# Kernel tuning notes

Measured on AMD Instinct MI355X. Metric: run time of the kernel, lower is better.

Reference implementation:

```python
import jax, jax.numpy as jnp
import numpy as np
from math import sqrt

B, NQ, NK = 16, 1024, 1024
DIM_Q = DIM_K = DIM_V = 512
H = 8
EPS = 1e-5


def _layernorm(x, gamma, beta):
    mu = jnp.mean(x, axis=-1, keepdims=True)
    var = jnp.mean(jnp.square(x - mu), axis=-1, keepdims=True)
    return (x - mu) * jax.lax.rsqrt(var + EPS) * gamma + beta


def setup_inputs() -> dict:
    key = jax.random.key(0)
    ks = jax.random.split(key, 12)
    s = 0.02
    return {
        "Q": jax.random.normal(ks[0], (B, NQ, DIM_Q), jnp.float32),
        "K": jax.random.normal(ks[1], (B, NK, DIM_K), jnp.float32),
        "Wq": jax.random.normal(ks[2], (DIM_Q, DIM_V), jnp.float32) * s,
        "bq": jnp.zeros((DIM_V,), jnp.float32),
        "Wk": jax.random.normal(ks[3], (DIM_K, DIM_V), jnp.float32) * s,
        "bk": jnp.zeros((DIM_V,), jnp.float32),
        "Wv": jax.random.normal(ks[4], (DIM_K, DIM_V), jnp.float32) * s,
        "bv": jnp.zeros((DIM_V,), jnp.float32),
        "Wo": jax.random.normal(ks[5], (DIM_V, DIM_V), jnp.float32) * s,
        "bo": jnp.zeros((DIM_V,), jnp.float32),
        "g0": jnp.ones((DIM_V,), jnp.float32),
        "b0": jnp.zeros((DIM_V,), jnp.float32),
        "g1": jnp.ones((DIM_V,), jnp.float32),
        "b1": jnp.zeros((DIM_V,), jnp.float32),
    }


def reference(Q, K, Wq, bq, Wk, bk, Wv, bv, Wo, bo, g0, b0, g1, b1):
    d = DIM_V // H  # head dim
    q = (Q @ Wq + bq).reshape(B, NQ, H, d)
    k = (K @ Wk + bk).reshape(B, NK, H, d)
    v = (K @ Wv + bv).reshape(B, NK, H, d)
    # NOTE: original scales by sqrt(dim_V), not sqrt(head_dim)
    scores = jnp.einsum("bqhd,bkhd->bhqk", q, k) / sqrt(DIM_V)
    A = jax.nn.softmax(scores, axis=-1)
    attn = jnp.einsum("bhqk,bkhd->bqhd", A, v)
    O = (q + attn).reshape(B, NQ, DIM_V)  # residual is post-projection q
    O = _layernorm(O, g0, b0)
    O = O + jax.nn.relu(O @ Wo + bo)
    O = _layernorm(O, g1, b1)
    return O
```

## Files before the change

### kernel.cpp

```cpp
#include <hip/hip_runtime.h>
#include <hip/hip_bf16.h>

typedef __attribute__((ext_vector_type(8))) short short8;
typedef __attribute__((ext_vector_type(4))) float f32x4;
typedef __attribute__((ext_vector_type(4))) float float4v;
typedef __attribute__((ext_vector_type(4))) unsigned short ushort4v;
typedef __attribute__((ext_vector_type(4))) unsigned int uint4v;
typedef __attribute__((ext_vector_type(2))) unsigned int uint2v;

#define MFMA16(a, b, c) __builtin_amdgcn_mfma_f32_16x16x32_bf16((a), (b), (c), 0, 0, 0)

__device__ __forceinline__ unsigned short f2bf(float f) {
    union { float f; unsigned u; } v; v.f = f;
    unsigned r = v.u + 0x7fffu + ((v.u >> 16) & 1u);
    return (unsigned short)(r >> 16);
}
__device__ __forceinline__ float bf2f(unsigned short h) {
    union { unsigned u; float f; } v; v.u = (unsigned)h << 16;
    return v.f;
}
__device__ __forceinline__ float asf(unsigned u) {
    union { unsigned u; float f; } v; v.u = u;
    return v.f;
}
__device__ __forceinline__ unsigned cvt_pk_bf16(float lo, float hi) {
    unsigned r;
    asm("v_cvt_pk_bf16_f32 %0, %1, %2" : "=v"(r) : "v"(lo), "v"(hi));
    return r;
}
__device__ __forceinline__ void gl16(const void* g, void* l) {
    __builtin_amdgcn_global_load_lds(
        (const __attribute__((address_space(1))) unsigned int*)g,
        (__attribute__((address_space(3))) unsigned int*)l, 16, 0, 0);
}

__global__ __launch_bounds__(256) void wtrans_kernel(
    const float* __restrict__ W0, const float* __restrict__ W1,
    const float* __restrict__ W2, const float* __restrict__ W3,
    unsigned short* __restrict__ T0, unsigned short* __restrict__ T1,
    unsigned short* __restrict__ T2, unsigned short* __restrict__ T3)
{
    const int z = blockIdx.z;
    const float* W = (z == 0) ? W0 : (z == 1) ? W1 : (z == 2) ? W2 : W3;
    unsigned short* T = (z == 0) ? T0 : (z == 1) ? T1 : (z == 2) ? T2 : T3;

    __shared__ unsigned short tile[64][72];
    const int k0 = blockIdx.x * 64, n0 = blockIdx.y * 64;
    const int t = threadIdx.x;

#pragma unroll
    for (int p = 0; p < 4; ++p) {
        int idx = p * 256 + t;
        int k = idx >> 4, c4 = idx & 15;
        float4v v = *(const float4v*)(W + (size_t)(k0 + k) * 512 + n0 + c4 * 4);
#pragma unroll
        for (int j = 0; j < 4; ++j) tile[k][c4 * 4 + j] = f2bf(v[j]);
    }
    __syncthreads();
#pragma unroll
    for (int p = 0; p < 2; ++p) {
        int idx = p * 256 + t;
        int n = idx >> 3, c = idx & 7;
        short8 o;
#pragma unroll
        for (int j = 0; j < 8; ++j) o[j] = (short)tile[c * 8 + j][n];
        *(short8*)(T + (size_t)(n0 + n) * 512 + k0 + ((c ^ (n & 7)) * 8)) = o;
    }
}

__global__ __launch_bounds__(256) void proj_kernel(
    const float* __restrict__ Q, const float* __restrict__ Kin,
    const unsigned short* __restrict__ WqT, const unsigned short* __restrict__ WkT,
    const unsigned short* __restrict__ WvT,
    const float* __restrict__ bq, const float* __restrict__ bk, const float* __restrict__ bv,
    unsigned short* __restrict__ qb, unsigned short* __restrict__ kb,
    unsigned short* __restrict__ vT)
{
    const int bid = blockIdx.x;
    const int xcd = bid & 7, idx = bid >> 3;
    const int q12 = idx / 12, combo = idx - q12 * 12;
    const int z = combo >> 2;
    const int rowbase = (xcd + 8 * q12) * 128;
    const int colbase = (combo & 3) * 128;

    const float* A = (z == 0) ? Q : Kin;
    const unsigned short* WT = (z == 0) ? WqT : (z == 1) ? WkT : WvT;
    const float* bias = (z == 0) ? bq : (z == 1) ? bk : bv;

    __shared__ float Alf[128 * 64];
    __shared__ unsigned short Bl[128 * 64];

    const int t = threadIdx.x;
    const int lane = t & 63, wid = t >> 6;
    const int wm = wid >> 1, wn = wid & 1;
    const int l15 = lane & 15, grp = lane >> 4;
    const int srow = t >> 3, sblk = t & 7;

    f32x4 acc[4][4];
#pragma unroll
    for (int i = 0; i < 4; ++i)
#pragma unroll
        for (int j = 0; j < 4; ++j) acc[i][j] = (f32x4){0.f, 0.f, 0.f, 0.f};

    for (int kt = 0; kt < 8; ++kt) {
#pragma unroll
        for (int p = 0; p < 4; ++p)
            gl16(WT + (size_t)(colbase + p * 32 + srow) * 512 + kt * 64 + sblk * 8,
                 &Bl[p * 2048 + wid * 512]);
#pragma unroll
        for (int i = 0; i < 8; ++i) {
            int r = wid * 32 + i * 4 + (lane >> 4);
            int cdst = lane & 15;
            gl16(A + (size_t)(rowbase + r) * 512 + kt * 64 + ((cdst ^ (r & 15)) << 2),
                 &Alf[wid * 2048 + i * 256]);
        }
        __syncthreads();
#pragma unroll
        for (int kk = 0; kk < 2; ++kk) {
            short8 af[4], bfr[4];
#pragma unroll
            for (int m = 0; m < 4; ++m) {
                int r = wm * 64 + m * 16 + l15;
                int c0 = kk * 8 + grp * 2;
                float4v f0 = *(const float4v*)((const char*)Alf + r * 256 + ((c0 ^ (r & 15)) << 4));
                float4v f1 = *(const float4v*)((const char*)Alf + r * 256 + (((c0 + 1) ^ (r & 15)) << 4));
                union { uint4v u; short8 s8; } cv;
                cv.u[0] = cvt_pk_bf16(f0[0], f0[1]);
                cv.u[1] = cvt_pk_bf16(f0[2], f0[3]);
                cv.u[2] = cvt_pk_bf16(f1[0], f1[1]);
                cv.u[3] = cvt_pk_bf16(f1[2], f1[3]);
                af[m] = cv.s8;
            }
#pragma unroll
            for (int n = 0; n < 4; ++n) {
                int r = wn * 64 + n * 16 + l15;
                bfr[n] = *(const short8*)((const char*)Bl + r * 128 + (((kk * 4 + grp) ^ (r & 7)) << 4));
            }
#pragma unroll
            for (int m = 0; m < 4; ++m)
#pragma unroll
                for (int n = 0; n < 4; ++n)
                    acc[m][n] = MFMA16(af[m], bfr[n], acc[m][n]);
        }
        __syncthreads();
    }

    if (z == 2) {
#pragma unroll
        for (int n = 0; n < 4; ++n) {
            int col = colbase + wn * 64 + n * 16 + l15;
            float bvv = bias[col];
            int h_ = col >> 6, d_ = col & 63;
#pragma unroll
            for (int m = 0; m < 4; ++m) {
                int row0 = rowbase + wm * 64 + m * 16 + grp * 4;
                int b_ = row0 >> 10;
                int key0 = row0 & 1023;
                int keypos = (key0 & ~63) + ((((key0 >> 3) & 7) ^ (d_ & 7)) << 3) + (key0 & 7);
                ushort4v w;
#pragma unroll
                for (int r = 0; r < 4; ++r) w[r] = f2bf(acc[m][n][r] + bvv);
                *(ushort4v*)(vT + ((size_t)(b_ * 8 + h_) * 64 + d_) * 1024 + keypos) = w;
            }
        }
    } else if (z == 1) {
#pragma unroll
        for (int n = 0; n < 4; ++n) {
            int col = colbase + wn * 64 + n * 16 + l15;
            float bvv = bias[col];
#pragma unroll
            for (int m = 0; m < 4; ++m) {
                int row0 = rowbase + wm * 64 + m * 16 + grp * 4;
#pragma unroll
                for (int r = 0; r < 4; ++r) {
                    int row = row0 + r;
                    int k6 = row & 63;
                    int y = ((k6 & 4) << 3) | ((k6 & 56) >> 1) | (k6 & 3);
                    int Y = (row & ~63) | y;
                    int colp = col ^ ((y & 7) << 3);
                    kb[(size_t)Y * 512 + colp] = f2bf(acc[m][n][r] + bvv);
                }
            }
        }
    } else {
#pragma unroll
        for (int n = 0; n < 4; ++n) {
            int col = colbase + wn * 64 + n * 16 + l15;
            float bvv = bias[col];
#pragma unroll
            for (int m = 0; m < 4; ++m) {
                int row0 = rowbase + wm * 64 + m * 16 + grp * 4;
#pragma unroll
                for (int r = 0; r < 4; ++r)
                    qb[(size_t)(row0 + r) * 512 + col] = f2bf(acc[m][n][r] + bvv);
            }
        }
    }
}

__global__ __launch_bounds__(256, 4) void attn_kernel(
    const unsigned short* __restrict__ qb, const unsigned short* __restrict__ kbs,
    const unsigned short* __restrict__ vTs, unsigned short* __restrict__ Opre)
{
    __shared__ unsigned short Kl[2][64 * 64];
    __shared__ unsigned short Vl[2][64 * 64];

    const int t = threadIdx.x, lane = t & 63, wid = t >> 6;
    const int l15 = lane & 15, grp = lane >> 4;

    const int bid = blockIdx.x;
    const int h = bid & 7, r2 = bid >> 3;
    const int b = r2 >> 3, qt = r2 & 7;
    const int qbase = qt * 128 + wid * 32;

    const unsigned short* ksrc = kbs + (size_t)(b * 1024 + (t >> 3)) * 512 + h * 64 + (t & 7) * 8;
    const unsigned short* vsrc = vTs + ((size_t)(b * 8 + h) * 64 + (t >> 3)) * 1024 + (t & 7) * 8;

#define STAGE(bsel, tile) do { \
    gl16(ksrc + (size_t)((tile) * 64) * 512,      &Kl[bsel][wid * 512]); \
    gl16(ksrc + (size_t)((tile) * 64 + 32) * 512, &Kl[bsel][2048 + wid * 512]); \
    gl16(vsrc + (tile) * 64,                      &Vl[bsel][wid * 512]); \
    gl16(vsrc + 32768 + (tile) * 64,              &Vl[bsel][2048 + wid * 512]); } while (0)

    const float C = 0.06375871f;

    short8 qfrag[2][2];
#pragma unroll
    for (int qf = 0; qf < 2; ++qf)
#pragma unroll
        for (int kk = 0; kk < 2; ++kk)
            qfrag[qf][kk] = *(const short8*)(
                qb + (size_t)(b * 1024 + qbase + qf * 16 + l15) * 512 + h * 64 + kk * 32 + grp * 8);

    STAGE(0, 0);

#pragma unroll
    for (int qf = 0; qf < 2; ++qf)
#pragma unroll
        for (int kk = 0; kk < 2; ++kk) {
            union { short8 s; uint4v u; } io;
            io.s = qfrag[qf][kk];
#pragma unroll
            for (int j = 0; j < 4; ++j) {
                unsigned w = io.u[j];
                float flo = asf(w << 16) * C;
                float fhi = asf(w & 0xffff0000u) * C;
                io.u[j] = cvt_pk_bf16(flo, fhi);
            }
            qfrag[qf][kk] = io.s;
        }

    f32x4 o[2][4];
#pragma unroll
    for (int qf = 0; qf < 2; ++qf)
#pragma unroll
        for (int df = 0; df < 4; ++df) o[qf][df] = (f32x4){0.f, 0.f, 0.f, 0.f};
    float mrun[2] = {0.f, 0.f}, lrun[2] = {0.f, 0.f};

    __syncthreads();

    for (int kt = 0; kt < 16; ++kt) {
        const int buf = kt & 1;
        if (kt < 15) STAGE(buf ^ 1, kt + 1);

        const char* Kb_ = (const char*)&Kl[buf][0];
        const char* Vb_ = (const char*)&Vl[buf][0];

        f32x4 s[2][4];
#pragma unroll
        for (int qf = 0; qf < 2; ++qf)
#pragma unroll
            for (int nf = 0; nf < 4; ++nf) s[qf][nf] = (f32x4){0.f, 0.f, 0.f, 0.f};
        __builtin_amdgcn_s_setprio(1);
#pragma unroll
        for (int kk = 0; kk < 2; ++kk) {
            short8 kf[4];
#pragma unroll
            for (int nf = 0; nf < 4; ++nf) {
                int r = nf * 16 + l15;
                kf[nf] = *(const short8*)(Kb_ + r * 128 + (((kk * 4 + grp) ^ (r & 7)) << 4));
            }
#pragma unroll
            for (int qf = 0; qf < 2; ++qf)
#pragma unroll
                for (int nf = 0; nf < 4; ++nf)
                    s[qf][nf] = MFMA16(kf[nf], qfrag[qf][kk], s[qf][nf]);
        }
        __builtin_amdgcn_s_setprio(0);

        short8 pa[2][2];
#pragma unroll
        for (int qf = 0; qf < 2; ++qf) {
            float a0 = fmaxf(fmaxf(s[qf][0][0], s[qf][0][1]), fmaxf(s[qf][0][2], s[qf][0][3]));
            float a1 = fmaxf(fmaxf(s[qf][1][0], s[qf][1][1]), fmaxf(s[qf][1][2], s[qf][1][3]));
            float a2 = fmaxf(fmaxf(s[qf][2][0], s[qf][2][1]), fmaxf(s[qf][2][2], s[qf][2][3]));
            float a3 = fmaxf(fmaxf(s[qf][3][0], s[qf][3][1]), fmaxf(s[qf][3][2], s[qf][3][3]));
            float lm = fmaxf(fmaxf(a0, a1), fmaxf(a2, a3));
            if (__any(lm - mrun[qf] > 8.f)) {
                float mr = lm;
                mr = fmaxf(mr, __shfl_xor(mr, 16));
                mr = fmaxf(mr, __shfl_xor(mr, 32));
                float mnew = fmaxf(mrun[qf], mr);
                float rs = __builtin_amdgcn_exp2f(mrun[qf] - mnew);
                mrun[qf] = mnew;
                lrun[qf] *= rs;
#pragma unroll
                for (int df = 0; df < 4; ++df)
#pragma unroll
                    for (int r = 0; r < 4; ++r) o[qf][df][r] *= rs;
            }
            float p[4][4];
            const float mq = mrun[qf];
            if (mq == 0.f) {
#pragma unroll
                for (int nf = 0; nf < 4; ++nf)
#pragma unroll
                    for (int r = 0; r < 4; ++r)
                        p[nf][r] = __builtin_amdgcn_exp2f(s[qf][nf][r]);
            } else {
#pragma unroll
                for (int nf = 0; nf < 4; ++nf)
#pragma unroll
                    for (int r = 0; r < 4; ++r)
                        p[nf][r] = __builtin_amdgcn_exp2f(s[qf][nf][r] - mq);
            }
            float t0 = (p[0][0] + p[0][1]) + (p[0][2] + p[0][3]);
            float t1 = (p[1][0] + p[1][1]) + (p[1][2] + p[1][3]);
            float t2 = (p[2][0] + p[2][1]) + (p[2][2] + p[2][3]);
            float t3 = (p[3][0] + p[3][1]) + (p[3][2] + p[3][3]);
            lrun[qf] += (t0 + t1) + (t2 + t3);
            union { uint4v u; short8 s8; } c0, c1;
            c0.u[0] = cvt_pk_bf16(p[0][0], p[0][1]);
            c0.u[1] = cvt_pk_bf16(p[0][2], p[0][3]);
            c0.u[2] = cvt_pk_bf16(p[2][0], p[2][1]);
            c0.u[3] = cvt_pk_bf16(p[2][2], p[2][3]);
            c1.u[0] = cvt_pk_bf16(p[1][0], p[1][1]);
            c1.u[1] = cvt_pk_bf16(p[1][2], p[1][3]);
            c1.u[2] = cvt_pk_bf16(p[3][0], p[3][1]);
            c1.u[3] = cvt_pk_bf16(p[3][2], p[3][3]);
            pa[qf][0] = c0.s8;
            pa[qf][1] = c1.s8;
        }

        __builtin_amdgcn_s_setprio(1);
#pragma unroll
        for (int kk = 0; kk < 2; ++kk)
#pragma unroll
            for (int df = 0; df < 4; ++df) {
                int r = df * 16 + l15;
                short8 vf = *(const short8*)(Vb_ + r * 128 + (((kk * 4 + grp) ^ (r & 7)) << 4));
#pragma unroll
                for (int qf = 0; qf < 2; ++qf)
                    o[qf][df] = MFMA16(vf, pa[qf][kk], o[qf][df]);
            }
        __builtin_amdgcn_s_setprio(0);
        __syncthreads();
    }
#undef STAGE

#pragma unroll
    for (int qf = 0; qf < 2; ++qf) {
        float l = lrun[qf];
        l += __shfl_xor(l, 16);
        l += __shfl_xor(l, 32);
        float linv = 1.f / l;
        size_t row = (size_t)(b * 1024 + qbase + qf * 16 + l15);
#pragma unroll
        for (int df = 0; df < 4; ++df) {
            int col = h * 64 + df * 16 + grp * 4;
            ushort4v res = *(const ushort4v*)(qb + row * 512 + col);
            ushort4v outv;
#pragma unroll
            for (int r = 0; r < 4; ++r)
                outv[r] = f2bf(o[qf][df][r] * linv + bf2f(res[r]));
            *(ushort4v*)(Opre + row * 512 + col) = outv;
        }
    }
}

template <int OUT_F32>
__global__ __launch_bounds__(256) void ln_kernel(
    const unsigned short* in, const float* __restrict__ g, const float* __restrict__ be,
    unsigned short* outb, float* outf)
{
    const int wid = threadIdx.x >> 6, lane = threadIdx.x & 63;
    const size_t row = (size_t)blockIdx.x * 4 + wid;
    short8 v = *(const short8*)(in + row * 512 + lane * 8);
    float x[8];
    float sum = 0.f, sq = 0.f;
#pragma unroll
    for (int j = 0; j < 8; ++j) {
        x[j] = bf2f((unsigned short)v[j]);
        sum += x[j];
        sq += x[j] * x[j];
    }
#pragma unroll
    for (int ofs = 1; ofs < 64; ofs <<= 1) {
        sum += __shfl_xor(sum, ofs);
        sq += __shfl_xor(sq, ofs);
    }
    float mean = sum * (1.f / 512.f);
    float var = sq * (1.f / 512.f) - mean * mean;
    float rs = rsqrtf(var + 1e-5f);
    float4v g0 = *(const float4v*)(g + lane * 8);
    float4v g1 = *(const float4v*)(g + lane * 8 + 4);
    float4v b0 = *(const float4v*)(be + lane * 8);
    float4v b1 = *(const float4v*)(be + lane * 8 + 4);
    float y[8];
#pragma unroll
    for (int j = 0; j < 4; ++j) y[j] = (x[j] - mean) * rs * g0[j] + b0[j];
#pragma unroll
    for (int j = 0; j < 4; ++j) y[4 + j] = (x[4 + j] - mean) * rs * g1[j] + b1[j];
    if (OUT_F32) {
        float4v o0, o1;
#pragma unroll
        for (int j = 0; j < 4; ++j) { o0[j] = y[j]; o1[j] = y[4 + j]; }
        *(float4v*)(outf + row * 512 + lane * 8) = o0;
        *(float4v*)(outf + row * 512 + lane * 8 + 4) = o1;
    } else {
        short8 o;
#pragma unroll
        for (int j = 0; j < 8; ++j) o[j] = (short)f2bf(y[j]);
        size_t op = row * 512 + (size_t)((lane >> 3) * 64 + (((lane & 7) ^ ((int)row & 7)) * 8));
        *(short8*)(outb + op) = o;
    }
}

__global__ __launch_bounds__(256) void ffn_kernel(
    const unsigned short* __restrict__ O1, const unsigned short* __restrict__ WoT,
    const float* __restrict__ bo, unsigned short* __restrict__ O2)
{
    __shared__ unsigned short Al[128 * 64];
    __shared__ unsigned short Bl[128 * 64];

    const int bid = blockIdx.x;
    const int xcd = bid & 7, idx = bid >> 3;
    const int rowbase = (xcd + 8 * (idx >> 2)) * 128;
    const int colbase = (idx & 3) * 128;

    const int t = threadIdx.x;
    const int lane = t & 63, wid = t >> 6;
    const int wm = wid >> 1, wn = wid & 1;
    const int l15 = lane & 15, grp = lane >> 4;
    const int srow = t >> 3, sblk = t & 7;

    f32x4 acc[4][4];
#pragma unroll
    for (int i = 0; i < 4; ++i)
#pragma unroll
        for (int j = 0; j < 4; ++j) acc[i][j] = (f32x4){0.f, 0.f, 0.f, 0.f};

    for (int kt = 0; kt < 8; ++kt) {
#pragma unroll
        for (int p = 0; p < 4; ++p)
            gl16(O1 + (size_t)(rowbase + p * 32 + srow) * 512 + kt * 64 + sblk * 8,
                 &Al[p * 2048 + wid * 512]);
#pragma unroll
        for (int p = 0; p < 4; ++p)
            gl16(WoT + (size_t)(colbase + p * 32 + srow) * 512 + kt * 64 + sblk * 8,
                 &Bl[p * 2048 + wid * 512]);
        __syncthreads();
#pragma unroll
        for (int kk = 0; kk < 2; ++kk) {
            short8 af[4], bfr[4];
#pragma unroll
            for (int m = 0; m < 4; ++m) {
                int r = wm * 64 + m * 16 + l15;
                af[m] = *(const short8*)((const char*)Al + r * 128 + (((kk * 4 + grp) ^ (r & 7)) << 4));
            }
#pragma unroll
            for (int n = 0; n < 4; ++n) {
                int r = wn * 64 + n * 16 + l15;
                bfr[n] = *(const short8*)((const char*)Bl + r * 128 + (((kk * 4 + grp) ^ (r & 7)) << 4));
            }
#pragma unroll
            for (int m = 0; m < 4; ++m)
#pragma unroll
                for (int n = 0; n < 4; ++n)
                    acc[m][n] = MFMA16(af[m], bfr[n], acc[m][n]);
        }
        __syncthreads();
    }
#pragma unroll
    for (int n = 0; n < 4; ++n) {
        int col = colbase + wn * 64 + n * 16 + l15;
        float bvv = bo[col];
#pragma unroll
        for (int m = 0; m < 4; ++m) {
            int row0 = rowbase + wm * 64 + m * 16 + grp * 4;
#pragma unroll
            for (int r = 0; r < 4; ++r) {
                size_t row = (size_t)(row0 + r);
                float val = fmaxf(acc[m][n][r] + bvv, 0.f);
                float resid = bf2f(O1[row * 512 + (col ^ (((int)row & 7) << 3))]);
                O2[row * 512 + col] = f2bf(resid + val);
            }
        }
    }
}

extern "C" void kernel_launch(void* const* d_in, const int* in_sizes, int n_in,
                              void* d_out, int out_size, void* d_ws, size_t ws_size,
                              hipStream_t stream)
{
    const float* Q   = (const float*)d_in[0];
    const float* Kin = (const float*)d_in[1];
    const float* Wq  = (const float*)d_in[2];
    const float* bq  = (const float*)d_in[3];
    const float* Wk  = (const float*)d_in[4];
    const float* bk  = (const float*)d_in[5];
    const float* Wv  = (const float*)d_in[6];
    const float* bv  = (const float*)d_in[7];
    const float* Wo  = (const float*)d_in[8];
    const float* bo  = (const float*)d_in[9];
    const float* g0  = (const float*)d_in[10];
    const float* b0  = (const float*)d_in[11];
    const float* g1  = (const float*)d_in[12];
    const float* b1  = (const float*)d_in[13];
    float* out = (float*)d_out;

    unsigned short* ws = (unsigned short*)d_ws;
    const size_t WSZ = 512 * 512;
    const size_t BIG = 16384 * 512;
    unsigned short* WqT  = ws;
    unsigned short* WkT  = WqT + WSZ;
    unsigned short* WvT  = WkT + WSZ;
    unsigned short* WoT  = WvT + WSZ;
    unsigned short* qb   = WoT + WSZ;
    unsigned short* kb   = qb + BIG;
    unsigned short* vT   = kb + BIG;
    unsigned short* Opre = vT + BIG;
    unsigned short* O2   = Opre + BIG;
    unsigned short* O1   = Opre;

    wtrans_kernel<<<dim3(8, 8, 4), 256, 0, stream>>>(Wq, Wk, Wv, Wo, WqT, WkT, WvT, WoT);
    proj_kernel<<<dim3(1536), 256, 0, stream>>>(Q, Kin, WqT, WkT, WvT, bq, bk, bv, qb, kb, vT);
    attn_kernel<<<dim3(1024), 256, 0, stream>>>(qb, kb, vT, Opre);
    ln_kernel<0><<<dim3(4096), 256, 0, stream>>>(Opre, g0, b0, O1, nullptr);
    ffn_kernel<<<dim3(512), 256, 0, stream>>>(O1, WoT, bo, O2);
    ln_kernel<1><<<dim3(4096), 256, 0, stream>>>(O2, g1, b1, nullptr, out);
}
```

Before: 136.5 us.

## Double-buffer LDS tiles in projection and FFN GEMMs with prefetch

The projection and FFN GEMM kernels now double-buffer their shared-memory tiles, prefetching the next K-tile while computing on the current one, and use one barrier per iteration instead of two. The projection kernel drops to a K-tile of 32 so the doubled fp32 A buffer fits, and the weight-transpose swizzle is changed to match the new 4-chunk-per-row B layout. MFMA blocks are wrapped in s_setprio to favour compute waves. The aim is to hide global-to-LDS load latency behind MFMA work, at the cost of more LDS per block, possibly lower occupancy, and more loop iterations in the projection kernel.

```diff
diff --git a/kernel.cpp b/kernel.cpp
--- a/kernel.cpp
+++ b/kernel.cpp
@@ -6,7 +6,6 @@
 typedef __attribute__((ext_vector_type(4))) float float4v;
 typedef __attribute__((ext_vector_type(4))) unsigned short ushort4v;
 typedef __attribute__((ext_vector_type(4))) unsigned int uint4v;
-typedef __attribute__((ext_vector_type(2))) unsigned int uint2v;
 
 #define MFMA16(a, b, c) __builtin_amdgcn_mfma_f32_16x16x32_bf16((a), (b), (c), 0, 0, 0)
 
@@ -64,7 +63,8 @@
         short8 o;
 #pragma unroll
         for (int j = 0; j < 8; ++j) o[j] = (short)tile[c * 8 + j][n];
-        *(short8*)(T + (size_t)(n0 + n) * 512 + k0 + ((c ^ (n & 7)) * 8)) = o;
+        int pos = (c & 4) | ((c ^ n) & 3);
+        *(short8*)(T + (size_t)(n0 + n) * 512 + k0 + pos * 8) = o;
     }
 }
 
@@ -87,14 +87,28 @@
     const unsigned short* WT = (z == 0) ? WqT : (z == 1) ? WkT : WvT;
     const float* bias = (z == 0) ? bq : (z == 1) ? bk : bv;
 
-    __shared__ float Alf[128 * 64];
-    __shared__ unsigned short Bl[128 * 64];
+    __shared__ float Alf[2][128 * 32];
+    __shared__ unsigned short Bl[2][128 * 32];
 
     const int t = threadIdx.x;
     const int lane = t & 63, wid = t >> 6;
     const int wm = wid >> 1, wn = wid & 1;
     const int l15 = lane & 15, grp = lane >> 4;
-    const int srow = t >> 3, sblk = t & 7;
+    const int arow = lane >> 3, achk = lane & 7;
+    const int brow = lane >> 2;
+
+#define PSTAGE(bsel, kt_) do { \
+    _Pragma("unroll") \
+    for (int i = 0; i < 4; ++i) { \
+        int r = wid * 32 + i * 8 + arow; \
+        gl16(A + (size_t)(rowbase + r) * 512 + (kt_) * 32 + ((achk ^ (r & 7)) << 2), \
+             &Alf[bsel][wid * 1024 + i * 256]); \
+    } \
+    _Pragma("unroll") \
+    for (int j = 0; j < 2; ++j) { \
+        gl16(WT + (size_t)(colbase + wid * 32 + j * 16 + brow) * 512 + (kt_) * 32 + (lane & 3) * 8, \
+             &Bl[bsel][wid * 1024 + j * 512]); \
+    } } while (0)
 
     f32x4 acc[4][4];
 #pragma unroll
@@ -102,48 +116,42 @@
 #pragma unroll
         for (int j = 0; j < 4; ++j) acc[i][j] = (f32x4){0.f, 0.f, 0.f, 0.f};
 
-    for (int kt = 0; kt < 8; ++kt) {
-#pragma unroll
-        for (int p = 0; p < 4; ++p)
-            gl16(WT + (size_t)(colbase + p * 32 + srow) * 512 + kt * 64 + sblk * 8,
-                 &Bl[p * 2048 + wid * 512]);
-#pragma unroll
-        for (int i = 0; i < 8; ++i) {
-            int r = wid * 32 + i * 4 + (lane >> 4);
-            int cdst = lane & 15;
-            gl16(A + (size_t)(rowbase + r) * 512 + kt * 64 + ((cdst ^ (r & 15)) << 2),
-                 &Alf[wid * 2048 + i * 256]);
-        }
+    PSTAGE(0, 0);
+    __syncthreads();
+
+    for (int kt = 0; kt < 16; ++kt) {
+        const int bsel = kt & 1;
+        if (kt < 15) PSTAGE(bsel ^ 1, kt + 1);
+
+        short8 af[4], bfr[4];
+#pragma unroll
+        for (int m = 0; m < 4; ++m) {
+            int r = wm * 64 + m * 16 + l15;
+            const char* base = (const char*)&Alf[bsel][0] + r * 128;
+            float4v f0 = *(const float4v*)(base + (((grp * 2) ^ (r & 7)) << 4));
+            float4v f1 = *(const float4v*)(base + (((grp * 2 + 1) ^ (r & 7)) << 4));
+            union { uint4v u; short8 s8; } cv;
+            cv.u[0] = cvt_pk_bf16(f0[0], f0[1]);
+            cv.u[1] = cvt_pk_bf16(f0[2], f0[3]);
+            cv.u[2] = cvt_pk_bf16(f1[0], f1[1]);
+            cv.u[3] = cvt_pk_bf16(f1[2], f1[3]);
+            af[m] = cv.s8;
+        }
+#pragma unroll
+        for (int n = 0; n < 4; ++n) {
+            int r = wn * 64 + n * 16 + l15;
+            bfr[n] = *(const short8*)((const char*)&Bl[bsel][0] + r * 64 + ((grp ^ (r & 3)) << 4));
+        }
+        __builtin_amdgcn_s_setprio(1);
+#pragma unroll
+        for (int m = 0; m < 4; ++m)
+#pragma unroll
+            for (int n = 0; n < 4; ++n)
+                acc[m][n] = MFMA16(af[m], bfr[n], acc[m][n]);
+        __builtin_amdgcn_s_setprio(0);
         __syncthreads();
-#pragma unroll
-        for (int kk = 0; kk < 2; ++kk) {
-            short8 af[4], bfr[4];
-#pragma unroll
-            for (int m = 0; m < 4; ++m) {
-                int r = wm * 64 + m * 16 + l15;
-                int c0 = kk * 8 + grp * 2;
-                float4v f0 = *(const float4v*)((const char*)Alf + r * 256 + ((c0 ^ (r & 15)) << 4));
-                float4v f1 = *(const float4v*)((const char*)Alf + r * 256 + (((c0 + 1) ^ (r & 15)) << 4));
-                union { uint4v u; short8 s8; } cv;
-                cv.u[0] = cvt_pk_bf16(f0[0], f0[1]);
-                cv.u[1] = cvt_pk_bf16(f0[2], f0[3]);
-                cv.u[2] = cvt_pk_bf16(f1[0], f1[1]);
-                cv.u[3] = cvt_pk_bf16(f1[2], f1[3]);
-                af[m] = cv.s8;
-            }
-#pragma unroll
-            for (int n = 0; n < 4; ++n) {
-                int r = wn * 64 + n * 16 + l15;
-                bfr[n] = *(const short8*)((const char*)Bl + r * 128 + (((kk * 4 + grp) ^ (r & 7)) << 4));
-            }
-#pragma unroll
-            for (int m = 0; m < 4; ++m)
-#pragma unroll
-                for (int n = 0; n < 4; ++n)
-                    acc[m][n] = MFMA16(af[m], bfr[n], acc[m][n]);
-        }
-        __syncthreads();
-    }
+    }
+#undef PSTAGE
 
     if (z == 2) {
 #pragma unroll
@@ -430,8 +438,8 @@
     const unsigned short* __restrict__ O1, const unsigned short* __restrict__ WoT,
     const float* __restrict__ bo, unsigned short* __restrict__ O2)
 {
-    __shared__ unsigned short Al[128 * 64];
-    __shared__ unsigned short Bl[128 * 64];
+    __shared__ unsigned short Al[2][128 * 64];
+    __shared__ unsigned short Bl[2][128 * 64];
 
     const int bid = blockIdx.x;
     const int xcd = bid & 7, idx = bid >> 3;
@@ -444,43 +452,52 @@
     const int l15 = lane & 15, grp = lane >> 4;
     const int srow = t >> 3, sblk = t & 7;
 
+#define FSTAGE(bsel, kt_) do { \
+    _Pragma("unroll") \
+    for (int p = 0; p < 4; ++p) { \
+        gl16(O1 + (size_t)(rowbase + p * 32 + srow) * 512 + (kt_) * 64 + sblk * 8, \
+             &Al[bsel][p * 2048 + wid * 512]); \
+        gl16(WoT + (size_t)(colbase + p * 32 + srow) * 512 + (kt_) * 64 + sblk * 8, \
+             &Bl[bsel][p * 2048 + wid * 512]); \
+    } } while (0)
+
     f32x4 acc[4][4];
 #pragma unroll
     for (int i = 0; i < 4; ++i)
 #pragma unroll
         for (int j = 0; j < 4; ++j) acc[i][j] = (f32x4){0.f, 0.f, 0.f, 0.f};
 
+    FSTAGE(0, 0);
+    __syncthreads();
+
     for (int kt = 0; kt < 8; ++kt) {
-#pragma unroll
-        for (int p = 0; p < 4; ++p)
-            gl16(O1 + (size_t)(rowbase + p * 32 + srow) * 512 + kt * 64 + sblk * 8,
-                 &Al[p * 2048 + wid * 512]);
-#pragma unroll
-        for (int p = 0; p < 4; ++p)
-            gl16(WoT + (size_t)(colbase + p * 32 + srow) * 512 + kt * 64 + sblk * 8,
-                 &Bl[p * 2048 + wid * 512]);
-        __syncthreads();
+        const int bsel = kt & 1;
+        if (kt < 7) FSTAGE(bsel ^ 1, kt + 1);
 #pragma unroll
         for (int kk = 0; kk < 2; ++kk) {
             short8 af[4], bfr[4];
 #pragma unroll
             for (int m = 0; m < 4; ++m) {
                 int r = wm * 64 + m * 16 + l15;
-                af[m] = *(const short8*)((const char*)Al + r * 128 + (((kk * 4 + grp) ^ (r & 7)) << 4));
+                af[m] = *(const short8*)((const char*)&Al[bsel][0] + r * 128 + (((kk * 4 + grp) ^ (r & 7)) << 4));
             }
 #pragma unroll
             for (int n = 0; n < 4; ++n) {
                 int r = wn * 64 + n * 16 + l15;
-                bfr[n] = *(const short8*)((const char*)Bl + r * 128 + (((kk * 4 + grp) ^ (r & 7)) << 4));
-            }
+                bfr[n] = *(const short8*)((const char*)&Bl[bsel][0] + r * 128 + (((kk * 4) | ((grp ^ r) & 3)) << 4));
+            }
+            __builtin_amdgcn_s_setprio(1);
 #pragma unroll
             for (int m = 0; m < 4; ++m)
 #pragma unroll
                 for (int n = 0; n < 4; ++n)
                     acc[m][n] = MFMA16(af[m], bfr[n], acc[m][n]);
+            __builtin_amdgcn_s_setprio(0);
         }
         __syncthreads();
     }
+#undef FSTAGE
+
 #pragma unroll
     for (int n = 0; n < 4; ++n) {
         int col = colbase + wn * 64 + n * 16 + l15;
```

Measured after the change: 146.3 us. 1.07x slower.
